# Kernel tuning notes

Hardware: AMD Instinct MI355X
Metric: run time of the kernel (lower is better)

The kernel has to match this reference:

```python
import jax, jax.numpy as jnp
import numpy as np

B, H, S, D = 4, 16, 1024, 64
MAX_REL = 16  # max_relative_position


def setup_inputs() -> dict:
    key = jax.random.key(0)
    kq, kk, kv, kr = jax.random.split(key, 4)
    Q = jax.random.normal(kq, (B, H, S, D), dtype=jnp.float32)
    K = jax.random.normal(kk, (B, H, S, D), dtype=jnp.float32)
    V = jax.random.normal(kv, (B, H, S, D), dtype=jnp.float32)
    # learned relative-position embedding table [2*P+1, d_k]
    rel_table = jax.random.normal(kr, (2 * MAX_REL + 1, D), dtype=jnp.float32) * 0.02
    # causal mask, broadcastable over batch/heads; 0 => masked
    mask = jnp.tril(jnp.ones((S, S), dtype=jnp.int32))[None, None, :, :]
    return {"Q": Q, "K": K, "V": V, "rel_table": rel_table, "mask": mask}


def reference(Q, K, V, rel_table, mask):
    scale = jnp.sqrt(jnp.asarray(Q.shape[-1], Q.dtype))
    seq_len = Q.shape[2]
    r = jnp.arange(seq_len)
    # clipped relative distances -> embedding indices in [0, 2P]
    idx = jnp.clip(r[None, :] - r[:, None], -MAX_REL, MAX_REL) + MAX_REL  # [S,S]
    rel_emb = rel_table[idx]  # [S, S, D]
    scores = jnp.einsum('bhld,bhrd->bhlr', Q, K) / scale  # [B,H,S,S]
    scores = scores + jnp.einsum('bhld,lrd->bhlr', Q, rel_emb)
    scores = jnp.where(mask == 0, -jnp.inf, scores)
    attn = jax.nn.softmax(scores, axis=-1)
    output = jnp.einsum('bhlr,bhrd->bhld', attn, V)  # [B,H,S,D]
    return (output, attn)
```

## Files before the change

### kernel.cpp

```cpp
#include <hip/hip_runtime.h>

#define S_ 1024
#define D_ 64
#define RT 16
#define SCP 1036

typedef _Float16 f16x4 __attribute__((ext_vector_type(4)));
typedef _Float16 f16x8 __attribute__((ext_vector_type(8)));
typedef __fp16  h16x2 __attribute__((ext_vector_type(2)));
typedef float f32x4 __attribute__((ext_vector_type(4)));

__global__ __launch_bounds__(256)
void prep_kv(const float* __restrict__ K, const float* __restrict__ V,
             _Float16* __restrict__ Kws, _Float16* __restrict__ VT) {
    if (blockIdx.x < 1024) {
        const int idx = blockIdx.x * 256 + threadIdx.x;
        const int g4  = idx & 3;
        const float* kp = K + (size_t)(idx >> 2) * 64 + g4 * 16;
        _Float16* dst = Kws + (size_t)(idx >> 2) * 64 + g4 * 16;
        f16x8 o0, o1;
        #pragma unroll
        for (int u = 0; u < 2; ++u) {
            float4 f0 = *reinterpret_cast<const float4*>(kp + 8 * u);
            float4 f1 = *reinterpret_cast<const float4*>(kp + 8 * u + 4);
            f16x8& o = u ? o1 : o0;
            o[0] = (_Float16)f0.x; o[1] = (_Float16)f0.y;
            o[2] = (_Float16)f0.z; o[3] = (_Float16)f0.w;
            o[4] = (_Float16)f1.x; o[5] = (_Float16)f1.y;
            o[6] = (_Float16)f1.z; o[7] = (_Float16)f1.w;
        }
        *reinterpret_cast<f16x8*>(dst)     = o0;
        *reinterpret_cast<f16x8*>(dst + 8) = o1;
    } else {
        const int idx = (blockIdx.x - 1024) * 256 + threadIdx.x;
        const int bh  = idx >> 12;
        const int kt  = (idx >> 6) & 63;
        const int col = idx & 63;
        const float* vp = V + ((size_t)bh * S_ + kt * 16) * D_ + col;
        _Float16* dst = VT + ((size_t)(bh * 64 + kt) * 64 + col) * 16;
        f16x8 a, b;
        #pragma unroll
        for (int kk = 0; kk < 16; ++kk) {
            float f = vp[(size_t)kk * D_];
            if (kk < 8) a[kk] = (_Float16)f; else b[kk - 8] = (_Float16)f;
        }
        *reinterpret_cast<f16x8*>(dst)     = a;
        *reinterpret_cast<f16x8*>(dst + 8) = b;
    }
}

__global__ __launch_bounds__(256, 4)
void relattn_main(const float* __restrict__ Q, const float* __restrict__ rel,
                  const _Float16* __restrict__ Kws, const _Float16* __restrict__ VT,
                  float* __restrict__ outO, float* outA) {
    __shared__ __align__(16) _Float16 sc[RT * SCP];
    __shared__ float qrel[RT * 17];
    __shared__ float rowsum[4][RT];

    const int tid  = threadIdx.x;
    const int lane = tid & 63;
    const int w    = tid >> 6;
    const int l15  = lane & 15;
    const int g4   = lane >> 4;
    const int bid  = blockIdx.x;
    const int bh   = (bid & 7) + 8 * (bid >> 9);
    const int tile = 63 - ((bid >> 3) & 63);
    const int R0   = tile * RT;
    const int nt16 = tile + 1;
    const int bound = 16 * nt16;

    const float* Qb = Q + (size_t)bh * S_ * D_;
    const _Float16* Kb = Kws + (size_t)bh * 64 * 1024;
    const _Float16* Vt = VT  + (size_t)bh * 64 * 1024;

    {
        const int mend = (bound + 255) & ~255;
        const f16x8 zz = {0, 0, 0, 0, 0, 0, 0, 0};
        const int r = tid >> 4;
        for (int c = bound + (tid & 15) * 8; c < mend; c += 128)
            *reinterpret_cast<f16x8*>(&sc[r * SCP + c]) = zz;
    }

    {
        int idx = tid;
        #pragma unroll
        for (int rep = 0; rep < 2; ++rep) {
            if (idx < RT * 17) {
                const int i = idx / 17;
                const int j = idx - i * 17;
                const float* qp = Qb + (size_t)(R0 + i) * D_;
                const float* rp = rel + j * D_;
                float s = 0.f;
                #pragma unroll
                for (int d = 0; d < D_; d += 4) {
                    float4 a = *reinterpret_cast<const float4*>(qp + d);
                    float4 b = *reinterpret_cast<const float4*>(rp + d);
                    s += a.x * b.x + a.y * b.y + a.z * b.z + a.w * b.w;
                }
                qrel[idx] = s;
            }
            idx = 256 + tid;
        }
    }

    f16x8 aq0, aq1;
    {
        const float* qp = Qb + (size_t)(R0 + l15) * D_ + 8 * g4;
        float4 f0 = *reinterpret_cast<const float4*>(qp);
        float4 f1 = *reinterpret_cast<const float4*>(qp + 4);
        float4 f2 = *reinterpret_cast<const float4*>(qp + 32);
        float4 f3 = *reinterpret_cast<const float4*>(qp + 36);
        aq0 = f16x8{(_Float16)(f0.x*0.125f), (_Float16)(f0.y*0.125f),
                    (_Float16)(f0.z*0.125f), (_Float16)(f0.w*0.125f),
                    (_Float16)(f1.x*0.125f), (_Float16)(f1.y*0.125f),
                    (_Float16)(f1.z*0.125f), (_Float16)(f1.w*0.125f)};
        aq1 = f16x8{(_Float16)(f2.x*0.125f), (_Float16)(f2.y*0.125f),
                    (_Float16)(f2.z*0.125f), (_Float16)(f2.w*0.125f),
                    (_Float16)(f3.x*0.125f), (_Float16)(f3.y*0.125f),
                    (_Float16)(f3.z*0.125f), (_Float16)(f3.w*0.125f)};
    }

    const int   myrow = R0 + l15;
    const float qr0v  = qrel[l15 * 17];
    const int fastmax = (R0 - 31) >> 4;

    float psum = 0.f;
    auto qk_load = [&](int ct, f16x8* kf) {
        const _Float16* kp = Kb + ((size_t)ct * 16 + l15) * 64 + 8 * g4;
        kf[0] = *reinterpret_cast<const f16x8*>(kp);
        kf[1] = *reinterpret_cast<const f16x8*>(kp + 32);
    };
    auto qk_load4 = [&](int ct0, f16x8* buf) {
        #pragma unroll
        for (int u = 0; u < 4; ++u)
            if (ct0 + 4 * u < nt16) qk_load(ct0 + 4 * u, buf + 2 * u);
    };

    f16x8 kA[8], kB[8];
    qk_load4(w, kA);

    __syncthreads();

    const float qr0 = qrel[l15 * 17];
    (void)qr0v;

    auto qk_compute = [&](int ct, const f16x8* kf) {
        f32x4 acc = {0.f, 0.f, 0.f, 0.f};
        acc = __builtin_amdgcn_mfma_f32_16x16x32_f16(kf[0], aq0, acc, 0, 0, 0);
        acc = __builtin_amdgcn_mfma_f32_16x16x32_f16(kf[1], aq1, acc, 0, 0, 0);
        float e[4];
        if (ct <= fastmax) {
            #pragma unroll
            for (int j = 0; j < 4; ++j) e[j] = __expf(acc[j] + qr0);
        } else {
            #pragma unroll
            for (int j = 0; j < 4; ++j) {
                const int dlt = myrow - (ct * 16 + 4 * g4 + j);
                e[j] = 0.f;
                if (dlt >= 0)
                    e[j] = __expf(acc[j] + ((dlt < 16) ? qrel[l15 * 17 + 16 - dlt]
                                                       : qr0));
            }
        }
        psum += (e[0] + e[1]) + (e[2] + e[3]);
        h16x2 lo = __builtin_amdgcn_cvt_pkrtz(e[0], e[1]);
        h16x2 hi = __builtin_amdgcn_cvt_pkrtz(e[2], e[3]);
        f16x4 pk = {(_Float16)lo[0], (_Float16)lo[1],
                    (_Float16)hi[0], (_Float16)hi[1]};
        *reinterpret_cast<f16x4*>(&sc[l15 * SCP + ct * 16 + 4 * g4]) = pk;
    };
    auto qk_compute4 = [&](int ct0, const f16x8* buf) {
        #pragma unroll
        for (int u = 0; u < 4; ++u)
            if (ct0 + 4 * u < nt16) qk_compute(ct0 + 4 * u, buf + 2 * u);
    };

    for (int ct0 = w; ct0 < nt16; ct0 += 32) {
        if (ct0 + 16 < nt16) qk_load4(ct0 + 16, kB);
        qk_compute4(ct0, kA);
        if (ct0 + 16 < nt16) {
            if (ct0 + 32 < nt16) qk_load4(ct0 + 32, kA);
            qk_compute4(ct0 + 16, kB);
        }
    }

    const int n0    = 16 * w;
    const int ktile = nt16;
    const int fg    = ktile >> 2;
    const int tail  = ktile & 3;
    const _Float16* vtb = Vt + ((size_t)(n0 + l15)) * 16 + 4 * g4;

    f16x4 bvA[4], bvB[4], bvC[4];
    auto pv_load = [&](int g, f16x4* bv) {
        #pragma unroll
        for (int u = 0; u < 4; ++u)
            bv[u] = *reinterpret_cast<const f16x4*>(vtb + (size_t)(4 * g + u) * 1024);
    };
    if (fg > 0) pv_load(0, bvA);
    if (fg > 1) pv_load(1, bvB);

    psum += __shfl_xor(psum, 16);
    psum += __shfl_xor(psum, 32);
    if (lane < 16) rowsum[w][lane] = psum;
    __syncthreads();

    f32x4 oa[4] = {{0,0,0,0},{0,0,0,0},{0,0,0,0},{0,0,0,0}};
    auto pv_mfma = [&](int g, const f16x4* bv) {
        #pragma unroll
        for (int u = 0; u < 4; ++u) {
            f16x4 ap = *reinterpret_cast<f16x4*>(
                &sc[l15 * SCP + (4 * g + u) * 16 + 4 * g4]);
            oa[u] = __builtin_amdgcn_mfma_f32_16x16x16f16(ap, bv[u], oa[u], 0, 0, 0);
        }
    };

    float* Ab = outA + ((size_t)bh * S_ + R0) * S_;
    #pragma unroll
    for (int ii = 0; ii < 4; ++ii) {
        const int i = 4 * w + ii;
        const float iv = 1.f / (rowsum[0][i] + rowsum[1][i] +
                                rowsum[2][i] + rowsum[3][i]);
        #pragma unroll
        for (int q = 0; q < 4; ++q) {
            const int c = q * 256 + lane * 4;
            f32x4 o = {0.f, 0.f, 0.f, 0.f};
            if (q * 256 < bound) {
                f16x4 sv = *reinterpret_cast<f16x4*>(&sc[i * SCP + c]);
                o = {(float)sv[0] * iv, (float)sv[1] * iv,
                     (float)sv[2] * iv, (float)sv[3] * iv};
            }
            __builtin_nontemporal_store(
                o, reinterpret_cast<f32x4*>(Ab + (size_t)i * S_ + c));
        }
    }

    if (fg > 2) pv_load(2, bvC);
    int g = 0;
    for (; g + 3 < fg; g += 3) {
        pv_mfma(g, bvA);
        pv_load(g + 3, bvA);
        pv_mfma(g + 1, bvB);
        if (g + 4 < fg) pv_load(g + 4, bvB);
        pv_mfma(g + 2, bvC);
        if (g + 5 < fg) pv_load(g + 5, bvC);
    }
    if (g < fg)     pv_mfma(g, bvA);
    if (g + 1 < fg) pv_mfma(g + 1, bvB);
    if (g + 2 < fg) pv_mfma(g + 2, bvC);

    for (int r = 0; r < tail; ++r) {
        const int kt = 4 * fg + r;
        f16x4 bv = *reinterpret_cast<const f16x4*>(vtb + (size_t)kt * 1024);
        f16x4 ap = *reinterpret_cast<f16x4*>(&sc[l15 * SCP + kt * 16 + 4 * g4]);
        oa[r] = __builtin_amdgcn_mfma_f32_16x16x16f16(ap, bv, oa[r], 0, 0, 0);
    }

    f32x4 op = (oa[0] + oa[1]) + (oa[2] + oa[3]);

    float* Ob = outO + (size_t)bh * S_ * D_;
    #pragma unroll
    for (int j = 0; j < 4; ++j) {
        const int row = 4 * g4 + j;
        const float s = rowsum[0][row] + rowsum[1][row] +
                        rowsum[2][row] + rowsum[3][row];
        Ob[(size_t)(R0 + row) * D_ + n0 + l15] = op[j] / s;
    }
}

extern "C" void kernel_launch(void* const* d_in, const int* in_sizes, int n_in,
                              void* d_out, int out_size, void* d_ws, size_t ws_size,
                              hipStream_t stream) {
    const float* Q   = (const float*)d_in[0];
    const float* K   = (const float*)d_in[1];
    const float* V   = (const float*)d_in[2];
    const float* rel = (const float*)d_in[3];

    float* out  = (float*)d_out;
    float* outO = out;
    float* outA = out + (size_t)4 * 16 * 1024 * 64;

    _Float16*  Kws  = (_Float16*)((char*)d_ws + (size_t)(1 << 20));
    _Float16*  VTws = (_Float16*)((char*)d_ws + (size_t)(10 << 20));

    prep_kv<<<dim3(2048), dim3(256), 0, stream>>>(K, V, Kws, VTws);
    relattn_main<<<dim3(4096), dim3(256), 0, stream>>>(Q, rel, Kws, VTws,
                                                       outO, outA);
}
```

Before: 122.9 us.

## Fuse PV MFMA into QK loop with per-wave partial outputs reduced in LDS

Each wave now computes P·V right after producing each 16-column score tile, using the packed fp16 probabilities in registers instead of rereading them from shared memory after a barrier. V tiles are prefetched alongside K tiles in the same double-buffered loop. Each wave covers all 64 output columns for its strided key tiles. The four per-wave partial outputs are then reduced through shared memory, which costs an extra barrier and more accumulator registers. The change is meant to remove the separate PV phase and its LDS reads, and to let PV MFMAs overlap with exp work.

```diff
diff --git a/kernel.cpp b/kernel.cpp
--- a/kernel.cpp
+++ b/kernel.cpp
@@ -120,31 +120,37 @@
                     (_Float16)(f3.z*0.125f), (_Float16)(f3.w*0.125f)};
     }
 
-    const int   myrow = R0 + l15;
-    const float qr0v  = qrel[l15 * 17];
+    const int myrow   = R0 + l15;
     const int fastmax = (R0 - 31) >> 4;
 
-    float psum = 0.f;
-    auto qk_load = [&](int ct, f16x8* kf) {
+    auto k_load = [&](int ct, f16x8* kf) {
         const _Float16* kp = Kb + ((size_t)ct * 16 + l15) * 64 + 8 * g4;
         kf[0] = *reinterpret_cast<const f16x8*>(kp);
         kf[1] = *reinterpret_cast<const f16x8*>(kp + 32);
     };
-    auto qk_load4 = [&](int ct0, f16x8* buf) {
-        #pragma unroll
-        for (int u = 0; u < 4; ++u)
-            if (ct0 + 4 * u < nt16) qk_load(ct0 + 4 * u, buf + 2 * u);
-    };
-
-    f16x8 kA[8], kB[8];
-    qk_load4(w, kA);
+    auto v_load = [&](int ct, f16x4* vf) {
+        const _Float16* vp = Vt + ((size_t)ct * 64 + l15) * 16 + 4 * g4;
+        #pragma unroll
+        for (int n = 0; n < 4; ++n)
+            vf[n] = *reinterpret_cast<const f16x4*>(vp + (size_t)n * 256);
+    };
+    auto load2 = [&](int ct0, f16x8* kf, f16x4* vf) {
+        k_load(ct0, kf);
+        v_load(ct0, vf);
+        if (ct0 + 4 < nt16) { k_load(ct0 + 4, kf + 2); v_load(ct0 + 4, vf + 4); }
+    };
+
+    f16x8 kA[4], kB[4];
+    f16x4 vA[8], vB[8];
+    load2(w, kA, vA);
 
     __syncthreads();
 
     const float qr0 = qrel[l15 * 17];
-    (void)qr0v;
-
-    auto qk_compute = [&](int ct, const f16x8* kf) {
+    float psum = 0.f;
+    f32x4 oa[4] = {{0,0,0,0},{0,0,0,0},{0,0,0,0},{0,0,0,0}};
+
+    auto comp_tile = [&](int ct, const f16x8* kf, const f16x4* vf) {
         f32x4 acc = {0.f, 0.f, 0.f, 0.f};
         acc = __builtin_amdgcn_mfma_f32_16x16x32_f16(kf[0], aq0, acc, 0, 0, 0);
         acc = __builtin_amdgcn_mfma_f32_16x16x32_f16(kf[1], aq1, acc, 0, 0, 0);
@@ -168,51 +174,28 @@
         f16x4 pk = {(_Float16)lo[0], (_Float16)lo[1],
                     (_Float16)hi[0], (_Float16)hi[1]};
         *reinterpret_cast<f16x4*>(&sc[l15 * SCP + ct * 16 + 4 * g4]) = pk;
-    };
-    auto qk_compute4 = [&](int ct0, const f16x8* buf) {
-        #pragma unroll
-        for (int u = 0; u < 4; ++u)
-            if (ct0 + 4 * u < nt16) qk_compute(ct0 + 4 * u, buf + 2 * u);
-    };
-
-    for (int ct0 = w; ct0 < nt16; ct0 += 32) {
-        if (ct0 + 16 < nt16) qk_load4(ct0 + 16, kB);
-        qk_compute4(ct0, kA);
-        if (ct0 + 16 < nt16) {
-            if (ct0 + 32 < nt16) qk_load4(ct0 + 32, kA);
-            qk_compute4(ct0 + 16, kB);
-        }
-    }
-
-    const int n0    = 16 * w;
-    const int ktile = nt16;
-    const int fg    = ktile >> 2;
-    const int tail  = ktile & 3;
-    const _Float16* vtb = Vt + ((size_t)(n0 + l15)) * 16 + 4 * g4;
-
-    f16x4 bvA[4], bvB[4], bvC[4];
-    auto pv_load = [&](int g, f16x4* bv) {
-        #pragma unroll
-        for (int u = 0; u < 4; ++u)
-            bv[u] = *reinterpret_cast<const f16x4*>(vtb + (size_t)(4 * g + u) * 1024);
-    };
-    if (fg > 0) pv_load(0, bvA);
-    if (fg > 1) pv_load(1, bvB);
+        #pragma unroll
+        for (int n = 0; n < 4; ++n)
+            oa[n] = __builtin_amdgcn_mfma_f32_16x16x16f16(pk, vf[n], oa[n], 0, 0, 0);
+    };
+    auto comp2 = [&](int ct0, const f16x8* kf, const f16x4* vf) {
+        comp_tile(ct0, kf, vf);
+        if (ct0 + 4 < nt16) comp_tile(ct0 + 4, kf + 2, vf + 4);
+    };
+
+    for (int c0 = w; c0 < nt16; c0 += 16) {
+        if (c0 + 8 < nt16) load2(c0 + 8, kB, vB);
+        comp2(c0, kA, vA);
+        if (c0 + 8 < nt16) {
+            if (c0 + 16 < nt16) load2(c0 + 16, kA, vA);
+            comp2(c0 + 8, kB, vB);
+        }
+    }
 
     psum += __shfl_xor(psum, 16);
     psum += __shfl_xor(psum, 32);
     if (lane < 16) rowsum[w][lane] = psum;
     __syncthreads();
-
-    f32x4 oa[4] = {{0,0,0,0},{0,0,0,0},{0,0,0,0},{0,0,0,0}};
-    auto pv_mfma = [&](int g, const f16x4* bv) {
-        #pragma unroll
-        for (int u = 0; u < 4; ++u) {
-            f16x4 ap = *reinterpret_cast<f16x4*>(
-                &sc[l15 * SCP + (4 * g + u) * 16 + 4 * g4]);
-            oa[u] = __builtin_amdgcn_mfma_f32_16x16x16f16(ap, bv[u], oa[u], 0, 0, 0);
-        }
-    };
 
     float* Ab = outA + ((size_t)bh * S_ + R0) * S_;
     #pragma unroll
@@ -234,36 +217,27 @@
         }
     }
 
-    if (fg > 2) pv_load(2, bvC);
-    int g = 0;
-    for (; g + 3 < fg; g += 3) {
-        pv_mfma(g, bvA);
-        pv_load(g + 3, bvA);
-        pv_mfma(g + 1, bvB);
-        if (g + 4 < fg) pv_load(g + 4, bvB);
-        pv_mfma(g + 2, bvC);
-        if (g + 5 < fg) pv_load(g + 5, bvC);
-    }
-    if (g < fg)     pv_mfma(g, bvA);
-    if (g + 1 < fg) pv_mfma(g + 1, bvB);
-    if (g + 2 < fg) pv_mfma(g + 2, bvC);
-
-    for (int r = 0; r < tail; ++r) {
-        const int kt = 4 * fg + r;
-        f16x4 bv = *reinterpret_cast<const f16x4*>(vtb + (size_t)kt * 1024);
-        f16x4 ap = *reinterpret_cast<f16x4*>(&sc[l15 * SCP + kt * 16 + 4 * g4]);
-        oa[r] = __builtin_amdgcn_mfma_f32_16x16x16f16(ap, bv, oa[r], 0, 0, 0);
-    }
-
-    f32x4 op = (oa[0] + oa[1]) + (oa[2] + oa[3]);
+    __syncthreads();
+
+    float* Opart = reinterpret_cast<float*>(sc);
+    #pragma unroll
+    for (int n = 0; n < 4; ++n)
+        #pragma unroll
+        for (int j = 0; j < 4; ++j)
+            Opart[((w * 16) + (4 * g4 + j)) * 64 + 16 * n + l15] = oa[n][j];
+    __syncthreads();
 
     float* Ob = outO + (size_t)bh * S_ * D_;
     #pragma unroll
-    for (int j = 0; j < 4; ++j) {
-        const int row = 4 * g4 + j;
+    for (int ii = 0; ii < 4; ++ii) {
+        const int row = 4 * w + ii;
         const float s = rowsum[0][row] + rowsum[1][row] +
                         rowsum[2][row] + rowsum[3][row];
-        Ob[(size_t)(R0 + row) * D_ + n0 + l15] = op[j] / s;
+        const float o = Opart[(0 * 16 + row) * 64 + lane] +
+                        Opart[(1 * 16 + row) * 64 + lane] +
+                        Opart[(2 * 16 + row) * 64 + lane] +
+                        Opart[(3 * 16 + row) * 64 + lane];
+        Ob[(size_t)(R0 + row) * D_ + lane] = o / s;
     }
 }
 
```

New measurement: 121.7 us. No clear change (-1.0%).
